# Kernel tuning notes

Measured on AMD Instinct MI355X. Metric: run time of the kernel, lower is better.

## Reference

```python
import jax, jax.numpy as jnp
import numpy as np
import math

INPUT_SIZE = 256
HIDDEN_SIZE = 1024
TIMESTEPS = 32768


def setup_inputs() -> dict:
    key = jax.random.key(0)
    ks = jax.random.split(key, 7)
    stdv = 1.0 / math.sqrt(HIDDEN_SIZE)
    u = lambda k, shape: jax.random.uniform(k, shape, jnp.float32, -stdv, stdv)
    return {
        "input_data": jax.random.normal(ks[0], (TIMESTEPS, 1, INPUT_SIZE), jnp.float32),
        "weight_ih": u(ks[1], (HIDDEN_SIZE, INPUT_SIZE)),
        "weight_hh": u(ks[2], (HIDDEN_SIZE, HIDDEN_SIZE)),
        "weight": u(ks[3], (HIDDEN_SIZE,)),
        "bias_ih": u(ks[4], (HIDDEN_SIZE,)),
        "bias_hh": u(ks[5], (HIDDEN_SIZE,)),
        "bias": u(ks[6], (HIDDEN_SIZE,)),
    }


def reference(input_data, weight_ih, weight_hh, weight, bias_ih, bias_hh, bias):
    # input_data: [T, 1, F] (batch must be 1, as in the original flatten-based matmuls)
    T, B, F = input_data.shape
    x = input_data.reshape(T, F)
    # Precompute all input projections as one GEMM: [T, H]
    xW = x @ weight_ih.T

    def step(h, xw):
        hW = weight_hh @ h  # [H]
        h_new = jnp.tanh(weight * xw * hW + bias_ih * xw + bias_hh * hW + bias)
        return h_new, h_new

    h0 = jnp.zeros((weight_hh.shape[0],), dtype=input_data.dtype)
    _, ys = jax.lax.scan(step, h0, xW)
    return ys[:, None, :]  # [T, 1, H]
```

## Files before the change

kernel.cpp:

```cpp
#include <hip/hip_runtime.h>
#include <hip/hip_bf16.h>
#include <stdint.h>

#define T_STEPS 32768
#define HID 1024
#define FIN 256
#define NB_SCAN 32
#define NB_HEAT 28
#define RPB 32
#define RPW 8
#define WORDS (HID / 2)

typedef unsigned long long ull;

__global__ __launch_bounds__(256) void gemm_xw(const float* __restrict__ x,
                                               const float* __restrict__ wih,
                                               float* __restrict__ out) {
    __shared__ float As[32][132];
    __shared__ float Bs[32][132];
    const int tid = threadIdx.x;
    const int m0 = blockIdx.y * 128;
    const int n0 = blockIdx.x * 128;
    const int tm = tid >> 4, tn = tid & 15;
    const int lr = tid >> 1, lc = (tid & 1) * 16;

    float acc[8][8];
#pragma unroll
    for (int i = 0; i < 8; ++i)
#pragma unroll
        for (int j = 0; j < 8; ++j) acc[i][j] = 0.f;

    for (int kk = 0; kk < FIN; kk += 32) {
#pragma unroll
        for (int u = 0; u < 4; ++u) {
            float4 av = *reinterpret_cast<const float4*>(
                &x[(size_t)(m0 + lr) * FIN + kk + lc + 4 * u]);
            float4 bv = *reinterpret_cast<const float4*>(
                &wih[(size_t)(n0 + lr) * FIN + kk + lc + 4 * u]);
            As[lc + 4 * u + 0][lr] = av.x;
            As[lc + 4 * u + 1][lr] = av.y;
            As[lc + 4 * u + 2][lr] = av.z;
            As[lc + 4 * u + 3][lr] = av.w;
            Bs[lc + 4 * u + 0][lr] = bv.x;
            Bs[lc + 4 * u + 1][lr] = bv.y;
            Bs[lc + 4 * u + 2][lr] = bv.z;
            Bs[lc + 4 * u + 3][lr] = bv.w;
        }
        __syncthreads();
#pragma unroll
        for (int k = 0; k < 32; ++k) {
            const float4* Ak = reinterpret_cast<const float4*>(&As[k][0]);
            const float4* Bk = reinterpret_cast<const float4*>(&Bs[k][0]);
            float4 a0 = Ak[tm * 2], a1 = Ak[tm * 2 + 1];
            float4 b0 = Bk[tn * 2], b1 = Bk[tn * 2 + 1];
            float a[8] = {a0.x, a0.y, a0.z, a0.w, a1.x, a1.y, a1.z, a1.w};
            float b[8] = {b0.x, b0.y, b0.z, b0.w, b1.x, b1.y, b1.z, b1.w};
#pragma unroll
            for (int i = 0; i < 8; ++i)
#pragma unroll
                for (int j = 0; j < 8; ++j) acc[i][j] = fmaf(a[i], b[j], acc[i][j]);
        }
        __syncthreads();
    }
#pragma unroll
    for (int i = 0; i < 8; ++i) {
        float4 o0 = make_float4(acc[i][0], acc[i][1], acc[i][2], acc[i][3]);
        float4 o1 = make_float4(acc[i][4], acc[i][5], acc[i][6], acc[i][7]);
        float* op = &out[(size_t)(m0 + tm * 8 + i) * HID + n0 + tn * 8];
        *reinterpret_cast<float4*>(op) = o0;
        *reinterpret_cast<float4*>(op + 4) = o1;
    }
}

__device__ __forceinline__ float fast_tanh(float x) {
    float cx = fminf(fmaxf(x, -16.f), 16.f);
    float e = __builtin_amdgcn_exp2f(cx * 2.8853900817779268f);
    return (e - 1.f) * __builtin_amdgcn_rcpf(e + 1.f);
}

__device__ __forceinline__ void poll8(const ull* __restrict__ src, int lane,
                                      ull (&v)[8]) {
#pragma unroll
    for (int i = 0; i < 8; ++i)
        v[i] = __hip_atomic_load(src + lane + 64 * i, __ATOMIC_RELAXED,
                                 __HIP_MEMORY_SCOPE_AGENT);
}

__device__ __forceinline__ bool check8(const ull (&v)[8], unsigned expb) {
    unsigned d = 0;
#pragma unroll
    for (int i = 0; i < 8; ++i) d |= (((unsigned)v[i]) ^ expb) & 0xFFu;
    return d == 0;
}

__device__ void heater_body(const int* quit, int tid) {
    float a0 = tid * 0.001f + 1.f, a1 = a0 + 1.f, a2 = a0 + 2.f, a3 = a0 + 3.f;
    float a4 = a0 + 4.f, a5 = a0 + 5.f, a6 = a0 + 6.f, a7 = a0 + 7.f;
    for (int it = 0; it < 300000; ++it) {
#pragma unroll 64
        for (int u = 0; u < 64; ++u) {
            a0 = fmaf(a0, 1.0000001f, 0.5f);
            a1 = fmaf(a1, 1.0000001f, 0.5f);
            a2 = fmaf(a2, 1.0000001f, 0.5f);
            a3 = fmaf(a3, 1.0000001f, 0.5f);
            a4 = fmaf(a4, 1.0000001f, 0.5f);
            a5 = fmaf(a5, 1.0000001f, 0.5f);
            a6 = fmaf(a6, 1.0000001f, 0.5f);
            a7 = fmaf(a7, 1.0000001f, 0.5f);
        }
        if (__hip_atomic_load(quit, __ATOMIC_RELAXED, __HIP_MEMORY_SCOPE_AGENT))
            break;
    }
    asm volatile("" ::"v"(a0), "v"(a1), "v"(a2), "v"(a3), "v"(a4), "v"(a5),
                 "v"(a6), "v"(a7));
}

__global__ __launch_bounds__(256, 1) void scan_rnn(
    const float* __restrict__ whh, const float* __restrict__ wgt,
    const float* __restrict__ bih, const float* __restrict__ bhh,
    const float* __restrict__ bb, float* __restrict__ out,
    ull* __restrict__ hbuf, int* __restrict__ quit) {
    if (blockIdx.x >= NB_SCAN) {
        heater_body(quit, threadIdx.x);
        return;
    }
    __shared__ ull hshw[WORDS];
    const int lane = threadIdx.x & 63;
    const int wv = threadIdx.x >> 6;
    const int r0 = blockIdx.x * RPB + wv * RPW;
    const int rr = r0 + (lane & 7);

    float wreg[RPW][16];
#pragma unroll
    for (int j = 0; j < RPW; ++j)
#pragma unroll
        for (int i = 0; i < 16; ++i)
            wreg[j][i] = whh[(size_t)(r0 + j) * HID + lane + 64 * i];

    const float cw = wgt[rr], cbi = bih[rr], cbh = bhh[rr], cb = bb[rr];
    float xw_cur = out[rr];

    for (int t = 0; t < T_STEPS; ++t) {
        if (wv == 0) {
            const ull* src =
                hbuf + ((size_t)(t & 1) * NB_SCAN + blockIdx.x) * WORDS;
            const unsigned expb = (unsigned)t & 0xFFu;
            ull va[8], vb[8];
            poll8(src, lane, va);
            for (;;) {
                poll8(src, lane, vb);
                if (check8(va, expb)) {
#pragma unroll
                    for (int i = 0; i < 8; ++i) hshw[lane + 64 * i] = va[i];
                    break;
                }
                poll8(src, lane, va);
                if (check8(vb, expb)) {
#pragma unroll
                    for (int i = 0; i < 8; ++i) hshw[lane + 64 * i] = vb[i];
                    break;
                }
                __builtin_amdgcn_s_sleep(1);
            }
        }
        __syncthreads();

        const float* hf = (const float*)(&hshw[0]);
        float hval[16];
#pragma unroll
        for (int i = 0; i < 16; ++i) hval[i] = hf[lane + 64 * i];

        float acc[RPW];
#pragma unroll
        for (int j = 0; j < RPW; ++j) acc[j] = 0.f;
#pragma unroll
        for (int i = 0; i < 16; ++i)
#pragma unroll
            for (int j = 0; j < RPW; ++j)
                acc[j] = fmaf(wreg[j][i], hval[i], acc[j]);

#pragma unroll
        for (int m = 1; m < 8; m <<= 1)
#pragma unroll
            for (int j = 0; j < RPW; ++j) acc[j] += __shfl_xor(acc[j], m, 64);
        float y = acc[0];
#pragma unroll
        for (int j = 1; j < RPW; ++j) y = ((lane & 7) == j) ? acc[j] : y;
#pragma unroll
        for (int m = 8; m < 64; m <<= 1) y += __shfl_xor(y, m, 64);

        const float arg = fmaf(fmaf(cw, xw_cur, cbh), y, fmaf(cbi, xw_cur, cb));
        const float hn = fast_tanh(arg);

        {
            const int j = lane & 3;
            const float lo_f = __shfl(hn, 2 * j, 8);
            const float hi_f = __shfl(hn, 2 * j + 1, 8);
            const unsigned tagb = (unsigned)(t + 1) & 0xFFu;
            const unsigned lo = (__float_as_uint(lo_f) & 0xFFFFFF00u) | tagb;
            const ull pv = ((ull)__float_as_uint(hi_f) << 32) | (ull)lo;
            const int widx = (r0 >> 1) + j;
            ull* dstbase =
                hbuf + (size_t)((t + 1) & 1) * NB_SCAN * WORDS + widx;
            const int cons = lane >> 2;
            __hip_atomic_store(dstbase + (size_t)cons * WORDS, pv,
                               __ATOMIC_RELAXED, __HIP_MEMORY_SCOPE_AGENT);
            __hip_atomic_store(dstbase + (size_t)(cons + 16) * WORDS, pv,
                               __ATOMIC_RELAXED, __HIP_MEMORY_SCOPE_AGENT);
        }
        if (lane < 8) out[(size_t)t * HID + rr] = hn;
        const int nt = t < T_STEPS - 1 ? t + 1 : t;
        xw_cur = out[(size_t)nt * HID + rr];
    }
    if (blockIdx.x == 0 && threadIdx.x == 0)
        __hip_atomic_store(quit, 1, __ATOMIC_RELAXED, __HIP_MEMORY_SCOPE_AGENT);
}

extern "C" void kernel_launch(void* const* d_in, const int* in_sizes, int n_in,
                              void* d_out, int out_size, void* d_ws, size_t ws_size,
                              hipStream_t stream) {
    const float* x = (const float*)d_in[0];
    const float* wih = (const float*)d_in[1];
    const float* whh = (const float*)d_in[2];
    const float* wgt = (const float*)d_in[3];
    const float* bih = (const float*)d_in[4];
    const float* bhh = (const float*)d_in[5];
    const float* bb = (const float*)d_in[6];
    float* out = (float*)d_out;

    ull* hbuf = (ull*)d_ws;
    const size_t hbytes = (size_t)2 * NB_SCAN * WORDS * sizeof(ull);
    int* quit = (int*)((char*)d_ws + hbytes);
    hipMemsetAsync(d_ws, 0, hbytes + 128, stream);

    dim3 ggrid(HID / 128, T_STEPS / 128);
    gemm_xw<<<ggrid, 256, 0, stream>>>(x, wih, out);

    scan_rnn<<<NB_SCAN + NB_HEAT, 256, 0, stream>>>(whh, wgt, bih, bhh, bb,
                                                    out, hbuf, quit);
}
```

Baseline: 64.70 ms.

## Have every wave poll the hidden-state buffer directly, dropping LDS staging and barrier

Measured after the change: 181.9 ms. 2.81x slower.

```diff
diff --git a/kernel.cpp b/kernel.cpp
--- a/kernel.cpp
+++ b/kernel.cpp
@@ -124,7 +124,6 @@
         heater_body(quit, threadIdx.x);
         return;
     }
-    __shared__ ull hshw[WORDS];
     const int lane = threadIdx.x & 63;
     const int wv = threadIdx.x >> 6;
     const int r0 = blockIdx.x * RPB + wv * RPW;
@@ -134,50 +133,41 @@
 #pragma unroll
     for (int j = 0; j < RPW; ++j)
 #pragma unroll
-        for (int i = 0; i < 16; ++i)
-            wreg[j][i] = whh[(size_t)(r0 + j) * HID + lane + 64 * i];
+        for (int i = 0; i < 8; ++i) {
+            wreg[j][2 * i + 0] = whh[(size_t)(r0 + j) * HID + 2 * (lane + 64 * i) + 0];
+            wreg[j][2 * i + 1] = whh[(size_t)(r0 + j) * HID + 2 * (lane + 64 * i) + 1];
+        }
 
     const float cw = wgt[rr], cbi = bih[rr], cbh = bhh[rr], cb = bb[rr];
     float xw_cur = out[rr];
 
     for (int t = 0; t < T_STEPS; ++t) {
-        if (wv == 0) {
-            const ull* src =
-                hbuf + ((size_t)(t & 1) * NB_SCAN + blockIdx.x) * WORDS;
-            const unsigned expb = (unsigned)t & 0xFFu;
-            ull va[8], vb[8];
+        const ull* src = hbuf + ((size_t)(t & 1) * NB_SCAN + blockIdx.x) * WORDS;
+        const unsigned expb = (unsigned)t & 0xFFu;
+        ull va[8], vb[8];
+        ull* hit;
+        poll8(src, lane, va);
+        for (;;) {
+            poll8(src, lane, vb);
+            if (check8(va, expb)) { hit = va; break; }
             poll8(src, lane, va);
-            for (;;) {
-                poll8(src, lane, vb);
-                if (check8(va, expb)) {
-#pragma unroll
-                    for (int i = 0; i < 8; ++i) hshw[lane + 64 * i] = va[i];
-                    break;
-                }
-                poll8(src, lane, va);
-                if (check8(vb, expb)) {
-#pragma unroll
-                    for (int i = 0; i < 8; ++i) hshw[lane + 64 * i] = vb[i];
-                    break;
-                }
-                __builtin_amdgcn_s_sleep(1);
+            if (check8(vb, expb)) { hit = vb; break; }
+            __builtin_amdgcn_s_sleep(1);
+        }
+
+        float acc[RPW];
+#pragma unroll
+        for (int j = 0; j < RPW; ++j) acc[j] = 0.f;
+#pragma unroll
+        for (int i = 0; i < 8; ++i) {
+            const float hlo = __uint_as_float((unsigned)hit[i]);
+            const float hhi = __uint_as_float((unsigned)(hit[i] >> 32));
+#pragma unroll
+            for (int j = 0; j < RPW; ++j) {
+                acc[j] = fmaf(wreg[j][2 * i + 0], hlo, acc[j]);
+                acc[j] = fmaf(wreg[j][2 * i + 1], hhi, acc[j]);
             }
         }
-        __syncthreads();
-
-        const float* hf = (const float*)(&hshw[0]);
-        float hval[16];
-#pragma unroll
-        for (int i = 0; i < 16; ++i) hval[i] = hf[lane + 64 * i];
-
-        float acc[RPW];
-#pragma unroll
-        for (int j = 0; j < RPW; ++j) acc[j] = 0.f;
-#pragma unroll
-        for (int i = 0; i < 16; ++i)
-#pragma unroll
-            for (int j = 0; j < RPW; ++j)
-                acc[j] = fmaf(wreg[j][i], hval[i], acc[j]);
 
 #pragma unroll
         for (int m = 1; m < 8; m <<= 1)
```
